# Optimization experiments

Hardware: AMD Instinct MI355X
Metric: run time of the kernel (lower is better)

## Reference

```python
import jax, jax.numpy as jnp
import numpy as np

NUM_BINS = 1025  # mask_max + 1, masks drawn from [0, 1024]


def setup_inputs() -> dict:
    key = jax.random.key(0)
    k1, k2, k3, k4 = jax.random.split(key, 4)
    H, W = 4096, 4096
    origin_density = jax.random.uniform(k1, (H, W), dtype=jnp.float32)
    pre_density = jax.random.uniform(k2, (H, W), dtype=jnp.float32)
    # ensure both masks share the same max (assert in the original module)
    origin_mask = jax.random.randint(k3, (H, W), 0, NUM_BINS, dtype=jnp.int32)
    new_mask = jax.random.randint(k4, (H, W), 0, NUM_BINS, dtype=jnp.int32)
    origin_mask = origin_mask.at[0, 0].set(NUM_BINS - 1)
    new_mask = new_mask.at[0, 0].set(NUM_BINS - 1)
    return {
        "origin_density": origin_density,
        "origin_mask": origin_mask,
        "pre_density": pre_density,
        "new_mask": new_mask,
    }


def _masked_histogram(density, mask):
    # weighted histogram: count[b] = sum of density where mask == b
    return jax.ops.segment_sum(density.reshape(-1), mask.reshape(-1),
                               num_segments=NUM_BINS)


def reference(origin_density, origin_mask, pre_density, new_mask):
    origin_count = _masked_histogram(origin_density, origin_mask)
    new_count = _masked_histogram(pre_density, new_mask)
    affine_loss = jnp.sum(jnp.abs(new_count - origin_count))
    return affine_loss
```

## Files before the change

### kernel.cpp

```cpp
#include <hip/hip_runtime.h>

#define NUM_BINS 1025
#define NBLK 512
#define BLOCK 256
#define SCALEF 1024.0f
#define INV_SCALE 0.0009765625f

__global__ __launch_bounds__(BLOCK) void hist_kernel(
    const float* __restrict__ od, const int* __restrict__ om,
    const float* __restrict__ pd, const int* __restrict__ nm,
    int* __restrict__ partial, int n, int nblk)
{
    __shared__ int lh[NUM_BINS];
    const int tid = threadIdx.x;
    for (int b = tid; b < NUM_BINS; b += BLOCK) lh[b] = 0;
    __syncthreads();

    const int n4 = n >> 2;
    const float4* od4 = (const float4*)od;
    const int4*   om4 = (const int4*)om;
    const float4* pd4 = (const float4*)pd;
    const int4*   nm4 = (const int4*)nm;

    const int stride = gridDim.x * BLOCK;
    int i = blockIdx.x * BLOCK + tid;
    if (i < n4) {
        float4 d = od4[i]; int4 m = om4[i];
        float4 e = pd4[i]; int4 q = nm4[i];
        for (;;) {
            const int j = i + stride;
            const bool more = j < n4;
            float4 d2, e2; int4 m2, q2;
            if (more) { d2 = od4[j]; m2 = om4[j]; e2 = pd4[j]; q2 = nm4[j]; }
            atomicAdd(&lh[m.x],  __float2int_rn(d.x * SCALEF));
            atomicAdd(&lh[m.y],  __float2int_rn(d.y * SCALEF));
            atomicAdd(&lh[m.z],  __float2int_rn(d.z * SCALEF));
            atomicAdd(&lh[m.w],  __float2int_rn(d.w * SCALEF));
            atomicAdd(&lh[q.x], -__float2int_rn(e.x * SCALEF));
            atomicAdd(&lh[q.y], -__float2int_rn(e.y * SCALEF));
            atomicAdd(&lh[q.z], -__float2int_rn(e.z * SCALEF));
            atomicAdd(&lh[q.w], -__float2int_rn(e.w * SCALEF));
            if (!more) break;
            d = d2; m = m2; e = e2; q = q2; i = j;
        }
    }
    if (blockIdx.x == 0 && tid == 0) {
        for (int k = n4 << 2; k < n; ++k) {
            atomicAdd(&lh[om[k]],  __float2int_rn(od[k] * SCALEF));
            atomicAdd(&lh[nm[k]], -__float2int_rn(pd[k] * SCALEF));
        }
    }
    __syncthreads();

    for (int b = tid; b < NUM_BINS; b += BLOCK)
        partial[b * nblk + (int)blockIdx.x] = lh[b];
}

__global__ __launch_bounds__(64) void reduce_kernel(
    const int* __restrict__ partial, float* __restrict__ out, int nblk)
{
    const int bin  = blockIdx.x;
    const int lane = threadIdx.x;
    int s = 0;
    for (int k = lane; k < nblk; k += 64)
        s += partial[bin * nblk + k];
    for (int off = 32; off > 0; off >>= 1)
        s += __shfl_down(s, off, 64);
    if (lane == 0)
        atomicAdd(out, fabsf((float)s) * INV_SCALE);
}

extern "C" void kernel_launch(void* const* d_in, const int* in_sizes, int n_in,
                              void* d_out, int out_size, void* d_ws, size_t ws_size,
                              hipStream_t stream) {
    const float* od = (const float*)d_in[0];
    const int*   om = (const int*)d_in[1];
    const float* pd = (const float*)d_in[2];
    const int*   nm = (const int*)d_in[3];
    float* out   = (float*)d_out;
    int* partial = (int*)d_ws;
    const int n = in_sizes[0];

    int nblk = NBLK;
    size_t need = (size_t)NUM_BINS * nblk * sizeof(int);
    if (need > ws_size) {
        nblk = (int)(ws_size / (NUM_BINS * sizeof(int)));
        if (nblk < 1) nblk = 1;
    }

    hipMemsetAsync(d_out, 0, sizeof(float), stream);
    hist_kernel<<<nblk, BLOCK, 0, stream>>>(od, om, pd, nm, partial, n, nblk);
    reduce_kernel<<<NUM_BINS, 64, 0, stream>>>(partial, out, nblk);
}
```

Measured before the change: 68.48 us.

## Merge per-block histograms with global atomics and quadruple grid size

```diff
diff --git a/kernel.cpp b/kernel.cpp
--- a/kernel.cpp
+++ b/kernel.cpp
@@ -1,7 +1,7 @@
 #include <hip/hip_runtime.h>
 
 #define NUM_BINS 1025
-#define NBLK 512
+#define NBLK 2048
 #define BLOCK 256
 #define SCALEF 1024.0f
 #define INV_SCALE 0.0009765625f
@@ -9,7 +9,7 @@
 __global__ __launch_bounds__(BLOCK) void hist_kernel(
     const float* __restrict__ od, const int* __restrict__ om,
     const float* __restrict__ pd, const int* __restrict__ nm,
-    int* __restrict__ partial, int n, int nblk)
+    int* __restrict__ bins_acc, int n)
 {
     __shared__ int lh[NUM_BINS];
     const int tid = threadIdx.x;
@@ -52,22 +52,34 @@
     }
     __syncthreads();
 
-    for (int b = tid; b < NUM_BINS; b += BLOCK)
-        partial[b * nblk + (int)blockIdx.x] = lh[b];
+    for (int b = tid; b < NUM_BINS; b += BLOCK) {
+        const int v = lh[b];
+        if (v != 0) atomicAdd(&bins_acc[b], v);
+    }
 }
 
-__global__ __launch_bounds__(64) void reduce_kernel(
-    const int* __restrict__ partial, float* __restrict__ out, int nblk)
+__global__ __launch_bounds__(1024) void final_kernel(
+    const int* __restrict__ bins_acc, float* __restrict__ out)
 {
-    const int bin  = blockIdx.x;
-    const int lane = threadIdx.x;
-    int s = 0;
-    for (int k = lane; k < nblk; k += 64)
-        s += partial[bin * nblk + k];
+    const int tid = threadIdx.x;
+    float v = 0.0f;
+    for (int b = tid; b < NUM_BINS; b += 1024)
+        v += fabsf((float)bins_acc[b]);
+
     for (int off = 32; off > 0; off >>= 1)
-        s += __shfl_down(s, off, 64);
-    if (lane == 0)
-        atomicAdd(out, fabsf((float)s) * INV_SCALE);
+        v += __shfl_down(v, off, 64);
+
+    __shared__ float wsum[16];
+    const int wave = tid >> 6;
+    const int lane = tid & 63;
+    if (lane == 0) wsum[wave] = v;
+    __syncthreads();
+    if (tid == 0) {
+        float t = 0.0f;
+        #pragma unroll
+        for (int w = 0; w < 16; ++w) t += wsum[w];
+        out[0] = t * INV_SCALE;
+    }
 }
 
 extern "C" void kernel_launch(void* const* d_in, const int* in_sizes, int n_in,
@@ -77,18 +89,11 @@
     const int*   om = (const int*)d_in[1];
     const float* pd = (const float*)d_in[2];
     const int*   nm = (const int*)d_in[3];
-    float* out   = (float*)d_out;
-    int* partial = (int*)d_ws;
+    float* out    = (float*)d_out;
+    int* bins_acc = (int*)d_ws;
     const int n = in_sizes[0];
 
-    int nblk = NBLK;
-    size_t need = (size_t)NUM_BINS * nblk * sizeof(int);
-    if (need > ws_size) {
-        nblk = (int)(ws_size / (NUM_BINS * sizeof(int)));
-        if (nblk < 1) nblk = 1;
-    }
-
-    hipMemsetAsync(d_out, 0, sizeof(float), stream);
-    hist_kernel<<<nblk, BLOCK, 0, stream>>>(od, om, pd, nm, partial, n, nblk);
-    reduce_kernel<<<NUM_BINS, 64, 0, stream>>>(partial, out, nblk);
+    hipMemsetAsync(bins_acc, 0, NUM_BINS * sizeof(int), stream);
+    hist_kernel<<<NBLK, BLOCK, 0, stream>>>(od, om, pd, nm, bins_acc, n);
+    final_kernel<<<1, 1024, 0, stream>>>(bins_acc, out);
 }
```

Result: slower. 70.51 us (+3.0%).
